# Optimization experiments

Measured on AMD Instinct MI355X. Metric: run time of the kernel, lower is better.

The kernel has to match this reference:

```python
import jax, jax.numpy as jnp
import numpy as np

N, D = 32, 16  # output capsules, output capsule dim
J, I = 16, 8   # input capsules, input capsule dim
B = 16384

def setup_inputs() -> dict:
    key = jax.random.key(0)
    k1, k2 = jax.random.split(key)
    inputs = jax.random.normal(k1, (B, J, I), dtype=jnp.float32)
    # kaiming_normal_ on (N,16,8,D): fan_in computed from dims -> std = sqrt(2/fan_in)
    fan_in = I * D  # torch fan_in for a 4D tensor (N,16,8,D) is dim1*receptive? faithful scale: gain*sqrt(1/fan)
    W = jax.random.normal(k2, (N, J, I, D), dtype=jnp.float32) * np.float32(np.sqrt(2.0 / (J * I * D / N if False else fan_in)))
    b = jnp.zeros((N, J, 1), dtype=jnp.float32)
    return {"inputs": inputs, "W": W, "b": b}

def reference(inputs, W, b):
    # pose transform: u[b,n,j,z] = sum_i inputs[b,j,i] * W[n,j,i,z]
    u = jnp.einsum('bji,njiz->bnjz', inputs, W)          # (B, N, J, D)
    # self-agreement: c[b,n,i] = sum_{k,j} u[b,n,i,j] * u[b,n,k,j]
    c = jnp.einsum('bnij,bnj->bni', u, u.sum(axis=-2))   # (B, N, J)
    c = c[..., None] / jnp.sqrt(jnp.float32(D))          # (B, N, J, 1)
    c = jax.nn.softmax(c, axis=1)                        # softmax over N axis (torch dim=1)
    c = c + b                                            # broadcast (N, J, 1)
    s = jnp.sum(u * c, axis=-2)                          # (B, N, D)
    return s
```

## Files before the change

### kernel.cpp

```cpp
#include <hip/hip_runtime.h>

#define B_TOT 16384
#define TBB   16
#define NTH   256
#define SLS   524

typedef short bf16x8 __attribute__((ext_vector_type(8)));
typedef float f32x4  __attribute__((ext_vector_type(4)));
union U4 { bf16x8 v; uint4 q; };

__device__ __forceinline__ unsigned f2bf(float f) {
    unsigned u = __float_as_uint(f);
    return (u + 0x7fffu + ((u >> 16) & 1u)) >> 16;
}

__device__ __forceinline__ uint4 packrow(const float* src) {
    uint4 o;
    o.x = f2bf(src[0])  | (f2bf(src[16])  << 16);
    o.y = f2bf(src[32]) | (f2bf(src[48])  << 16);
    o.z = f2bf(src[64]) | (f2bf(src[80])  << 16);
    o.w = f2bf(src[96]) | (f2bf(src[112]) << 16);
    return o;
}

__global__ void prepack(const float* __restrict__ W, uint4* __restrict__ Wp)
{
    const int t = blockIdx.x * 256 + threadIdx.x;
    const int lane = t & 63, s = (t >> 6) & 3, n = t >> 8;
    const int q = lane >> 4, z = lane & 15;
    Wp[t] = packrow(W + (size_t)(n * 16 + 4 * s + q) * 128 + z);
}

__global__ __launch_bounds__(NTH, 4)
void caps(const float* __restrict__ X, const uint4* __restrict__ Wp,
          const float* __restrict__ Bias, float* __restrict__ Out)
{
    __shared__ __align__(16) float sL[TBB * SLS];
    __shared__ float sBias[512];

    const int t    = threadIdx.x;
    const int lane = t & 63;
    const int wv   = t >> 6;
    const int b16  = lane & 15;
    const int q    = lane >> 4;
    const long bb  = (long)blockIdx.x * TBB;

    sBias[t]       = Bias[t];
    sBias[t + 256] = Bias[t + 256];

    unsigned moct[4];
    #pragma unroll
    for (int c = 0; c < 4; ++c) moct[c] = (q == c) ? 0xffffffffu : 0u;

    uint4 xq[4];
    #pragma unroll
    for (int s = 0; s < 4; ++s) {
        const float* xs = X + (bb + b16) * 128 + (4 * s + q) * 8;
        float4 a = *reinterpret_cast<const float4*>(xs);
        float4 c = *reinterpret_cast<const float4*>(xs + 4);
        uint4 o;
        o.x = f2bf(a.x) | (f2bf(a.y) << 16);
        o.y = f2bf(a.z) | (f2bf(a.w) << 16);
        o.z = f2bf(c.x) | (f2bf(c.y) << 16);
        o.w = f2bf(c.z) | (f2bf(c.w) << 16);
        xq[s] = o;
    }

    const f32x4 zero4 = {0.f, 0.f, 0.f, 0.f};

    auto maskA = [&](const uint4& wkf, int c) {
        U4 a;
        const unsigned m = moct[c];
        a.q.x = wkf.x & m; a.q.y = wkf.y & m;
        a.q.z = wkf.z & m; a.q.w = wkf.w & m;
        return a;
    };

    uint4 wk[4], wn[4];

    {
        const uint4* p0 = Wp + (wv * 8) * 256 + lane;
        wk[0] = p0[0]; wk[1] = p0[64]; wk[2] = p0[128]; wk[3] = p0[192];
    }
    #pragma unroll 1
    for (int nq = 0; nq < 8; ++nq) {
        const int n  = wv * 8 + nq;
        const int np = (nq < 7) ? n + 1 : n;
        const uint4* pn = Wp + np * 256 + lane;
        wn[0] = pn[0]; wn[1] = pn[64]; wn[2] = pn[128]; wn[3] = pn[192];

        f32x4 usum = zero4;
        #pragma unroll
        for (int s = 0; s < 4; ++s) {
            U4 a;  a.q  = wk[s];
            U4 xb; xb.q = xq[s];
            usum = __builtin_amdgcn_mfma_f32_16x16x32_bf16(a.v, xb.v, usum, 0, 0, 0);
        }

        float lv[16];
        #pragma unroll
        for (int j = 0; j < 16; ++j) {
            U4 a  = maskA(wk[j >> 2], j & 3);
            U4 xb; xb.q = xq[j >> 2];
            f32x4 u = __builtin_amdgcn_mfma_f32_16x16x32_bf16(a.v, xb.v, zero4, 0, 0, 0);
            float p = u[0] * usum[0];
            p = fmaf(u[1], usum[1], p);
            p = fmaf(u[2], usum[2], p);
            p = fmaf(u[3], usum[3], p);
            p += __shfl_xor(p, 16);
            p += __shfl_xor(p, 32);
            lv[j] = p * 0.25f;
        }
        if (lane < 16) {
            float4* dst = reinterpret_cast<float4*>(&sL[b16 * SLS + n * 16]);
            dst[0] = make_float4(lv[0],  lv[1],  lv[2],  lv[3]);
            dst[1] = make_float4(lv[4],  lv[5],  lv[6],  lv[7]);
            dst[2] = make_float4(lv[8],  lv[9],  lv[10], lv[11]);
            dst[3] = make_float4(lv[12], lv[13], lv[14], lv[15]);
        }
        wk[0] = wn[0]; wk[1] = wn[1]; wk[2] = wn[2]; wk[3] = wn[3];
    }
    __syncthreads();

    {
        const int sb = t >> 4, sj = t & 15;
        float l[32];
        #pragma unroll
        for (int n = 0; n < 32; ++n) l[n] = sL[sb * SLS + n * 16 + sj];
        float m = l[0];
        #pragma unroll
        for (int n = 1; n < 32; ++n) m = fmaxf(m, l[n]);
        float Z = 0.f;
        #pragma unroll
        for (int n = 0; n < 32; ++n) { l[n] = __expf(l[n] - m); Z += l[n]; }
        const float inv = 1.0f / Z;
        #pragma unroll
        for (int n = 0; n < 32; ++n)
            sL[sb * SLS + n * 16 + sj] = fmaf(l[n], inv, sBias[n * 16 + sj]);
    }
    __syncthreads();

    {
        const uint4* p0 = Wp + (wv * 8) * 256 + lane;
        wk[0] = p0[0]; wk[1] = p0[64]; wk[2] = p0[128]; wk[3] = p0[192];
    }
    #pragma unroll 1
    for (int nq = 0; nq < 8; ++nq) {
        const int n  = wv * 8 + nq;
        const int np = (nq < 7) ? n + 1 : n;
        const uint4* pn = Wp + np * 256 + lane;
        wn[0] = pn[0]; wn[1] = pn[64]; wn[2] = pn[128]; wn[3] = pn[192];

        float s0 = 0.f, s1 = 0.f, s2 = 0.f, s3 = 0.f;
        #pragma unroll
        for (int jp = 0; jp < 8; ++jp) {
            float2 c2 = *reinterpret_cast<const float2*>(&sL[b16 * SLS + n * 16 + 2 * jp]);
            U4 a0 = maskA(wk[jp >> 1], (2 * jp) & 3);
            U4 a1 = maskA(wk[jp >> 1], (2 * jp + 1) & 3);
            U4 x0; x0.q = xq[jp >> 1];
            f32x4 u0 = __builtin_amdgcn_mfma_f32_16x16x32_bf16(a0.v, x0.v, zero4, 0, 0, 0);
            f32x4 u1 = __builtin_amdgcn_mfma_f32_16x16x32_bf16(a1.v, x0.v, zero4, 0, 0, 0);
            s0 = fmaf(c2.x, u0[0], s0); s0 = fmaf(c2.y, u1[0], s0);
            s1 = fmaf(c2.x, u0[1], s1); s1 = fmaf(c2.y, u1[1], s1);
            s2 = fmaf(c2.x, u0[2], s2); s2 = fmaf(c2.y, u1[2], s2);
            s3 = fmaf(c2.x, u0[3], s3); s3 = fmaf(c2.y, u1[3], s3);
        }
        float4* op = reinterpret_cast<float4*>(Out + (bb + b16) * 512 + n * 16 + q * 4);
        *op = make_float4(s0, s1, s2, s3);
        wk[0] = wn[0]; wk[1] = wn[1]; wk[2] = wn[2]; wk[3] = wn[3];
    }
}

extern "C" void kernel_launch(void* const* d_in, const int* in_sizes, int n_in,
                              void* d_out, int out_size, void* d_ws, size_t ws_size,
                              hipStream_t stream) {
    const float* X  = (const float*)d_in[0];
    const float* W  = (const float*)d_in[1];
    const float* Bi = (const float*)d_in[2];
    float* Out = (float*)d_out;

    uint4* Wp = (uint4*)d_ws;
    prepack<<<32, 256, 0, stream>>>(W, Wp);
    caps<<<B_TOT / TBB, NTH, 0, stream>>>(X, Wp, Bi, Out);
}
```

Measured before the change: 101.7 us.

## Double threads per block, split capsules across eight waves, drop W prefetch

The block grows from 4 to 8 waves, so each wave handles 4 output capsules instead of 8. The register double-buffer prefetch of the next capsule's weights is removed, and logits are stored to LDS in groups of four instead of being buffered as 16 values. Together these lower register pressure and raise wave-level parallelism. In exchange, weight-load latency is no longer hidden by software prefetch, and the softmax phase uses only half the threads. The launch bound now asks for 8 blocks of 512 threads, which the ~34 KB of LDS per block cannot fit.

```diff
diff --git a/kernel.cpp b/kernel.cpp
--- a/kernel.cpp
+++ b/kernel.cpp
@@ -2,7 +2,7 @@
 
 #define B_TOT 16384
 #define TBB   16
-#define NTH   256
+#define NTH   512
 #define SLS   524
 
 typedef short bf16x8 __attribute__((ext_vector_type(8)));
@@ -31,7 +31,7 @@
     Wp[t] = packrow(W + (size_t)(n * 16 + 4 * s + q) * 128 + z);
 }
 
-__global__ __launch_bounds__(NTH, 4)
+__global__ __launch_bounds__(NTH, 8)
 void caps(const float* __restrict__ X, const uint4* __restrict__ Wp,
           const float* __restrict__ Bias, float* __restrict__ Out)
 {
@@ -45,8 +45,7 @@
     const int q    = lane >> 4;
     const long bb  = (long)blockIdx.x * TBB;
 
-    sBias[t]       = Bias[t];
-    sBias[t + 256] = Bias[t + 256];
+    sBias[t] = Bias[t];
 
     unsigned moct[4];
     #pragma unroll
@@ -76,18 +75,13 @@
         return a;
     };
 
-    uint4 wk[4], wn[4];
+    uint4 wk[4];
 
-    {
-        const uint4* p0 = Wp + (wv * 8) * 256 + lane;
-        wk[0] = p0[0]; wk[1] = p0[64]; wk[2] = p0[128]; wk[3] = p0[192];
-    }
     #pragma unroll 1
-    for (int nq = 0; nq < 8; ++nq) {
-        const int n  = wv * 8 + nq;
-        const int np = (nq < 7) ? n + 1 : n;
-        const uint4* pn = Wp + np * 256 + lane;
-        wn[0] = pn[0]; wn[1] = pn[64]; wn[2] = pn[128]; wn[3] = pn[192];
+    for (int nq = 0; nq < 4; ++nq) {
+        const int n = wv * 4 + nq;
+        const uint4* pw = Wp + n * 256 + lane;
+        wk[0] = pw[0]; wk[1] = pw[64]; wk[2] = pw[128]; wk[3] = pw[192];
 
         f32x4 usum = zero4;
         #pragma unroll
@@ -97,7 +91,7 @@
             usum = __builtin_amdgcn_mfma_f32_16x16x32_bf16(a.v, xb.v, usum, 0, 0, 0);
         }
 
-        float lv[16];
+        float lv[4];
         #pragma unroll
         for (int j = 0; j < 16; ++j) {
             U4 a  = maskA(wk[j >> 2], j & 3);
@@ -109,20 +103,15 @@
             p = fmaf(u[3], usum[3], p);
             p += __shfl_xor(p, 16);
             p += __shfl_xor(p, 32);
-            lv[j] = p * 0.25f;
+            lv[j & 3] = p * 0.25f;
+            if ((j & 3) == 3 && lane < 16)
+                *reinterpret_cast<float4*>(&sL[b16 * SLS + n * 16 + (j - 3)]) =
+                    make_float4(lv[0], lv[1], lv[2], lv[3]);
         }
-        if (lane < 16) {
-            float4* dst = reinterpret_cast<float4*>(&sL[b16 * SLS + n * 16]);
-            dst[0] = make_float4(lv[0],  lv[1],  lv[2],  lv[3]);
-            dst[1] = make_float4(lv[4],  lv[5],  lv[6],  lv[7]);
-            dst[2] = make_float4(lv[8],  lv[9],  lv[10], lv[11]);
-            dst[3] = make_float4(lv[12], lv[13], lv[14], lv[15]);
-        }
-        wk[0] = wn[0]; wk[1] = wn[1]; wk[2] = wn[2]; wk[3] = wn[3];
     }
     __syncthreads();
 
-    {
+    if (t < 256) {
         const int sb = t >> 4, sj = t & 15;
         float l[32];
         #pragma unroll
@@ -140,16 +129,11 @@
     }
     __syncthreads();
 
-    {
-        const uint4* p0 = Wp + (wv * 8) * 256 + lane;
-        wk[0] = p0[0]; wk[1] = p0[64]; wk[2] = p0[128]; wk[3] = p0[192];
-    }
     #pragma unroll 1
-    for (int nq = 0; nq < 8; ++nq) {
-        const int n  = wv * 8 + nq;
-        const int np = (nq < 7) ? n + 1 : n;
-        const uint4* pn = Wp + np * 256 + lane;
-        wn[0] = pn[0]; wn[1] = pn[64]; wn[2] = pn[128]; wn[3] = pn[192];
+    for (int nq = 0; nq < 4; ++nq) {
+        const int n = wv * 4 + nq;
+        const uint4* pw = Wp + n * 256 + lane;
+        wk[0] = pw[0]; wk[1] = pw[64]; wk[2] = pw[128]; wk[3] = pw[192];
 
         float s0 = 0.f, s1 = 0.f, s2 = 0.f, s3 = 0.f;
         #pragma unroll
@@ -167,7 +151,6 @@
         }
         float4* op = reinterpret_cast<float4*>(Out + (bb + b16) * 512 + n * 16 + q * 4);
         *op = make_float4(s0, s1, s2, s3);
-        wk[0] = wn[0]; wk[1] = wn[1]; wk[2] = wn[2]; wk[3] = wn[3];
     }
 }
 
```

Measured after the change: 107.0 us. 1.05x slower.
